# Optimization experiments

Hardware: AMD Instinct MI355X
Metric: run time of the kernel (lower is better)

## Reference

```python
import jax, jax.numpy as jnp
import numpy as np

N_NODES = 50000
N_EDGES = 800000
LATENT = 64
K_STEPS = 2
GAMMA = 0.9


def _xavier(key, fan_in, fan_out):
    lim = float(np.sqrt(6.0 / (fan_in + fan_out)))
    return jax.random.uniform(key, (fan_in, fan_out), minval=-lim, maxval=lim, dtype=jnp.float32)


def setup_inputs() -> dict:
    key = jax.random.key(0)
    ks = iter(jax.random.split(key, 48))
    L = LATENT
    inp = {}
    inp["x"] = jax.random.normal(next(ks), (N_NODES, 1), dtype=jnp.float32)
    inp["sol"] = jax.random.normal(next(ks), (N_NODES, 1), dtype=jnp.float32)
    inp["y"] = jax.random.normal(next(ks), (N_NODES, 1), dtype=jnp.float32)
    inp["tags"] = jax.random.randint(next(ks), (N_NODES,), 0, 2, dtype=jnp.int32)
    inp["edge_index"] = jax.random.randint(next(ks), (2, N_EDGES), 0, N_NODES, dtype=jnp.int32)
    inp["edge_attr"] = jax.random.normal(next(ks), (N_EDGES, 3), dtype=jnp.float32)
    inp["a_ij"] = jax.random.normal(next(ks), (N_EDGES,), dtype=jnp.float32)
    inp["prb_data"] = jax.random.normal(next(ks), (N_NODES, 2), dtype=jnp.float32)
    # phi_to / phi_from message MLPs: (2L+3) -> L -> L
    for name in ("pt", "pf"):
        inp[name + "_W1"] = _xavier(next(ks), 2 * L + 3, L)
        inp[name + "_b1"] = jnp.zeros((L,), jnp.float32)
        inp[name + "_W2"] = _xavier(next(ks), L, L)
        inp[name + "_b2"] = jnp.zeros((L,), jnp.float32)
    # gating MLPs: (3L+2) -> L, single linear + activation
    for name in ("zk", "rk", "corr"):
        inp[name + "_W"] = _xavier(next(ks), 3 * L + 2, L)
        inp[name + "_b"] = jnp.zeros((L,), jnp.float32)
    # encoder: 1 -> L -> L ; decoder: L -> L -> 1
    inp["e_W1"] = _xavier(next(ks), 1, L); inp["e_b1"] = jnp.zeros((L,), jnp.float32)
    inp["e_W2"] = _xavier(next(ks), L, L); inp["e_b2"] = jnp.zeros((L,), jnp.float32)
    inp["d_W1"] = _xavier(next(ks), L, L); inp["d_b1"] = jnp.zeros((L,), jnp.float32)
    inp["d_W2"] = _xavier(next(ks), L, 1); inp["d_b2"] = jnp.zeros((1,), jnp.float32)
    return inp


def reference(x, sol, y, tags, edge_index, edge_attr, a_ij, prb_data,
              pt_W1, pt_b1, pt_W2, pt_b2, pf_W1, pf_b1, pf_W2, pf_b2,
              zk_W, zk_b, rk_W, rk_b, corr_W, corr_b,
              e_W1, e_b1, e_W2, e_b2, d_W1, d_b1, d_W2, d_b2):
    n = x.shape[0]
    row, col = edge_index[0], edge_index[1]
    # remove_self_loops: mask out edges with row == col instead of slicing
    loop_mask = (row != col).astype(x.dtype)[:, None]

    def mlp2(t, W1, b1, W2, b2):  # Linear -> ReLU -> Linear
        return jnp.maximum(t @ W1 + b1, 0.0) @ W2 + b2

    def phi(h, i_idx, j_idx, W1, b1, W2, b2):
        # message = MLP([x_i, x_j, edge_attr]); aggr='add' at node i
        tmp = jnp.concatenate([h[i_idx], h[j_idx], edge_attr], axis=1)
        msg = mlp2(tmp, W1, b1, W2, b2) * loop_mask
        return jax.ops.segment_sum(msg, i_idx, num_segments=n)

    enc_p = (e_W1, e_b1, e_W2, e_b2)
    dec_p = (d_W1, d_b1, d_W2, d_b2)

    def apply(u, p):
        return mlp2(u, *p)

    def residual_loss(u):
        Au = jax.ops.segment_sum(a_ij[:, None] * u[col], row, num_segments=n)
        return jnp.mean((Au - y) ** 2)

    mse = lambda a, b: jnp.mean((a - b) ** 2)
    sg = lambda p: tuple(jax.lax.stop_gradient(t) for t in p)
    dir_mask = (tags == 1)[:, None]

    H0 = apply(x, enc_p)
    H = H0
    U = x
    total = jnp.float32(0.0)
    for step in range(K_STEPS):
        # phi_to: flow source->target => i = col (target); phi_from: i = row (source)
        mess_to = phi(H, col, row, pt_W1, pt_b1, pt_W2, pt_b2)
        mess_from = phi(H, row, col, pf_W1, pf_b1, pf_W2, pf_b2)
        cat = jnp.concatenate([H, mess_to, mess_from, prb_data], axis=1)
        alpha = jax.nn.sigmoid(cat @ zk_W + zk_b)
        reset = jax.nn.sigmoid(cat @ rk_W + rk_b)
        corr = jnp.tanh(
            jnp.concatenate([reset * H, mess_to, mess_from, prb_data], axis=1) @ corr_W + corr_b)
        Hn = H + alpha * corr
        Hn = jnp.where(dir_mask, H0, Hn)  # Dirichlet nodes reset to H['0']
        U = apply(Hn, dec_p)
        res = residual_loss(U)
        enc_loss = mse(apply(apply(Hn, sg(dec_p)), enc_p), Hn)        # 'latent'
        autoenc_loss = mse(apply(apply(U, sg(enc_p)), dec_p), U)      # 'physics'
        total = total + res * GAMMA ** (K_STEPS - step - 1) + enc_loss + autoenc_loss
        H = Hn
    return (U, total)
```

## Files before the change

### kernel.cpp

```cpp
#include <hip/hip_runtime.h>

#define DEV __device__ __forceinline__

constexpr int N = 50000;
constexpr int E = 800000;
constexpr int NBUK = 196;

constexpr int HF_OFF  = 0;
constexpr int H0F_OFF = 64*N;
constexpr int MTF_OFF = 128*N;
constexpr int MFF_OFF = 160*N;
constexpr int PBT_OFF = MTF_OFF;
constexpr int PBF_OFF = MFF_OFF;
constexpr int MP_OFF  = MTF_OFF;
constexpr int R1_OFF  = 192*N;
constexpr int PAT_OFF = R1_OFF;
constexpr int PAF_OFF = R1_OFF + 64*N;
constexpr int AL_OFF  = R1_OFF;
constexpr int RH_OFF  = R1_OFF + 64*N;
constexpr int T1_OFF  = R1_OFF;
constexpr int EV_OFF  = R1_OFF + 64*N;
constexpr int CSTG_OFF = R1_OFF;
constexpr int RSTG_OFF = R1_OFF + 4*E;
constexpr int HB_OFF   = 352*N;
constexpr int UV_OFF   = 384*N;
constexpr int LOSS_OFF = UV_OFF + N;
constexpr int FLAG_OFF = LOSS_OFF + 7;
constexpr int WZR_OFF = LOSS_OFF + 8;
constexpr int GB_OFF  = WZR_OFF + 24832;
constexpr int CW_OFF  = GB_OFF + 128;
constexpr int CB_OFF  = CW_OFF + 12416;
constexpr int PT1_OFF = CB_OFF + 64;
constexpr int AT_OFF  = PT1_OFF + 8192;
constexpr int BT1_OFF = AT_OFF + 192;
constexpr int WT2_OFF = BT1_OFF + 64;
constexpr int BT2_OFF = WT2_OFF + 4096;
constexpr int PF1_OFF = BT2_OFF + 64;
constexpr int AF_OFF  = PF1_OFF + 8192;
constexpr int BF1_OFF = AF_OFF + 192;
constexpr int WF2_OFF = BF1_OFF + 64;
constexpr int BF2_OFF = WF2_OFF + 4096;
constexpr int DW1_OFF = BF2_OFF + 64;
constexpr int DW2_OFF = DW1_OFF + 4096;
constexpr int DB1_OFF = DW2_OFF + 64;
constexpr int DB2_OFF = DB1_OFF + 64;
constexpr int EW1_OFF = DB2_OFF + 4;
constexpr int EB1_OFF = EW1_OFF + 64;
constexpr int EW2_OFF = EB1_OFF + 64;
constexpr int EB2_OFF = EW2_OFF + 4096;
constexpr int PRB0_OFF = EB2_OFF + 64;
constexpr int PRB1_OFF = PRB0_OFF + N;
constexpr int NWZR_OFF = PRB1_OFF + N;
constexpr int NCW_OFF  = NWZR_OFF + 25088;
constexpr int CNT_OFF  = NCW_OFF + 12544;
constexpr int FEND     = CNT_OFF + 2*N;
constexpr int CREC_OFF = FEND;
constexpr int RREC_OFF = CREC_OFF + 2*E;
constexpr int LCP_OFF  = RREC_OFF + 4*E;
constexpr int FRP_OFF  = LCP_OFF + N + 1;
constexpr int LE_OFF   = FRP_OFF + N + 1;
constexpr int LCF_OFF  = LE_OFF + N;
constexpr int LRF_OFF  = LCF_OFF + N;
constexpr int SFF_OFF  = LRF_OFF + N;
constexpr int CDEG_OFF = SFF_OFF + N;
constexpr int RDEG_OFF = CDEG_OFF + N;
constexpr int SDEG_OFF = RDEG_OFF + N;
constexpr int BS_OFF   = SDEG_OFF + N;
constexpr int BO_OFF   = BS_OFF + 512;
constexpr int GFC_OFF  = BO_OFF + 512;
constexpr int GFR_OFF  = GFC_OFF + 196;
constexpr int BKC_OFF  = GFR_OFF + 196;
constexpr int BKR_OFF  = BKC_OFF + 196;
constexpr int GBC_OFF  = BKR_OFF + 196;
constexpr int GBR_OFF  = GBC_OFF + 197;

constexpr int PREP_TOTAL = 24832+128+12416+64+8192+192+64+4096+64+8192+192+64+4096+64+4096+64+64+1+64+64+4096+64+6;
constexpr int PREP2_TOTAL = 25088 + 12544;

DEV float b2f(unsigned short u){ return __uint_as_float(((unsigned)u) << 16); }
DEV unsigned short f2b(float f){
    unsigned u = __float_as_uint(f);
    return (unsigned short)((u + 0x7fffu + ((u >> 16) & 1u)) >> 16);
}
DEV float blo(unsigned u){ return __uint_as_float(u << 16); }
DEV float bhi(unsigned u){ return __uint_as_float(u & 0xffff0000u); }
DEV int bcasti(int v, int k){ return __builtin_amdgcn_readlane(v, k); }
DEV float wave_sum(float v){
    #pragma unroll
    for (int off = 32; off > 0; off >>= 1) v += __shfl_xor(v, off, 64);
    return v;
}
DEV float ldv(const void* p, int i, bool isbf){
    return isbf ? b2f(((const unsigned short*)p)[i]) : ((const float*)p)[i];
}
DEV unsigned short ld16(const void* p, int i, bool isbf){
    return isbf ? ((const unsigned short*)p)[i] : f2b(((const float*)p)[i]);
}
DEV float sigm(float x){ return 1.f / (1.f + __expf(-x)); }

struct WPtrs {
    const void *ptW1, *ptb1, *ptW2, *ptb2;
    const void *pfW1, *pfb1, *pfW2, *pfb2;
    const void *zkW, *zkb, *rkW, *rkb, *cW, *cb;
    const void *eW1, *eb1, *eW2, *eb2;
    const void *dW1, *db1, *dW2, *db2;
};

__global__ __launch_bounds__(256) void detect_kernel(const void* y, float* __restrict__ ws){
    __shared__ int bad;
    if (threadIdx.x == 0) bad = 0;
    __syncthreads();
    const unsigned short* yy = (const unsigned short*)y;
    int mybad = 0;
    for (int i = threadIdx.x; i < 4096; i += 256){
        float v = b2f(yy[i]);
        if (!(v > -1.0e6f && v < 1.0e6f)) mybad = 1;
    }
    if (mybad) bad = 1;
    __syncthreads();
    if (threadIdx.x == 0) ws[FLAG_OFF] = bad ? 0.0f : 1.0f;
}

__global__ __launch_bounds__(256) void prep_kernel(WPtrs P, float* __restrict__ ws){
    int j = blockIdx.x * 256 + threadIdx.x;
    if (j >= PREP_TOTAL) return;
    bool isbf = ws[FLAG_OFF] > 0.5f;
    if (j < 24832){
        int k = j >> 7, c = j & 127;
        ws[WZR_OFF+j] = (c < 64) ? ldv(P.zkW, k*64+c, isbf) : ldv(P.rkW, k*64+(c-64), isbf);
        return;
    } j -= 24832;
    if (j < 128){ ws[GB_OFF+j] = (j < 64) ? ldv(P.zkb, j, isbf) : ldv(P.rkb, j-64, isbf); return; } j -= 128;
    if (j < 12416){ ws[CW_OFF+j] = ldv(P.cW, j, isbf); return; } j -= 12416;
    if (j < 64){ ws[CB_OFF+j] = ldv(P.cb, j, isbf); return; } j -= 64;
    if (j < 8192){ ws[PT1_OFF+j] = ldv(P.ptW1, j, isbf); return; } j -= 8192;
    if (j < 192){ ws[AT_OFF+j] = ldv(P.ptW1, 128*64+j, isbf); return; } j -= 192;
    if (j < 64){ ws[BT1_OFF+j] = ldv(P.ptb1, j, isbf); return; } j -= 64;
    if (j < 4096){ ws[WT2_OFF+j] = ldv(P.ptW2, j, isbf); return; } j -= 4096;
    if (j < 64){ ws[BT2_OFF+j] = ldv(P.ptb2, j, isbf); return; } j -= 64;
    if (j < 8192){ ws[PF1_OFF+j] = ldv(P.pfW1, j, isbf); return; } j -= 8192;
    if (j < 192){ ws[AF_OFF+j] = ldv(P.pfW1, 128*64+j, isbf); return; } j -= 192;
    if (j < 64){ ws[BF1_OFF+j] = ldv(P.pfb1, j, isbf); return; } j -= 64;
    if (j < 4096){ ws[WF2_OFF+j] = ldv(P.pfW2, j, isbf); return; } j -= 4096;
    if (j < 64){ ws[BF2_OFF+j] = ldv(P.pfb2, j, isbf); return; } j -= 64;
    if (j < 4096){ ws[DW1_OFF+j] = ldv(P.dW1, j, isbf); return; } j -= 4096;
    if (j < 64){ ws[DW2_OFF+j] = ldv(P.dW2, j, isbf); return; } j -= 64;
    if (j < 64){ ws[DB1_OFF+j] = ldv(P.db1, j, isbf); return; } j -= 64;
    if (j < 1){ ws[DB2_OFF] = ldv(P.db2, 0, isbf); return; } j -= 1;
    if (j < 64){ ws[EW1_OFF+j] = ldv(P.eW1, j, isbf); return; } j -= 64;
    if (j < 64){ ws[EB1_OFF+j] = ldv(P.eb1, j, isbf); return; } j -= 64;
    if (j < 4096){ ws[EW2_OFF+j] = ldv(P.eW2, j, isbf); return; } j -= 4096;
    if (j < 64){ ws[EB2_OFF+j] = ldv(P.eb2, j, isbf); return; } j -= 64;
    ws[LOSS_OFF+j] = 0.f;
}

__global__ __launch_bounds__(256) void prep2_kernel(float* __restrict__ ws){
    int j = blockIdx.x * 256 + threadIdx.x;
    if (j >= PREP2_TOTAL) return;
    if (j < 25088){
        int r = j >> 7, c = j & 127;
        float v;
        if (r < 64) v = ws[WZR_OFF + r*128 + c];
        else if (r < 128){
            int h = r - 64; float s = 0.f;
            for (int m = 0; m < 64; m++)
                s = fmaf(ws[WT2_OFF + h*64 + m], ws[WZR_OFF + (64+m)*128 + c], s);
            v = s;
        } else if (r < 192){
            int h = r - 128; float s = 0.f;
            for (int m = 0; m < 64; m++)
                s = fmaf(ws[WF2_OFF + h*64 + m], ws[WZR_OFF + (128+m)*128 + c], s);
            v = s;
        } else if (r < 194) v = ws[WZR_OFF + r*128 + c];
        else if (r == 194){
            float s = 0.f;
            for (int m = 0; m < 64; m++)
                s = fmaf(ws[BT2_OFF + m], ws[WZR_OFF + (64+m)*128 + c], s);
            v = s;
        } else {
            float s = 0.f;
            for (int m = 0; m < 64; m++)
                s = fmaf(ws[BF2_OFF + m], ws[WZR_OFF + (128+m)*128 + c], s);
            v = s;
        }
        ws[NWZR_OFF + j] = v;
        return;
    }
    j -= 25088;
    {
        int r = j >> 6, c = j & 63;
        float v;
        if (r < 64) v = ws[CW_OFF + r*64 + c];
        else if (r < 128){
            int h = r - 64; float s = 0.f;
            for (int m = 0; m < 64; m++)
                s = fmaf(ws[WT2_OFF + h*64 + m], ws[CW_OFF + (64+m)*64 + c], s);
            v = s;
        } else if (r < 192){
            int h = r - 128; float s = 0.f;
            for (int m = 0; m < 64; m++)
                s = fmaf(ws[WF2_OFF + h*64 + m], ws[CW_OFF + (128+m)*64 + c], s);
            v = s;
        } else if (r < 194) v = ws[CW_OFF + r*64 + c];
        else if (r == 194){
            float s = 0.f;
            for (int m = 0; m < 64; m++)
                s = fmaf(ws[BT2_OFF + m], ws[CW_OFF + (64+m)*64 + c], s);
            v = s;
        } else {
            float s = 0.f;
            for (int m = 0; m < 64; m++)
                s = fmaf(ws[BF2_OFF + m], ws[CW_OFF + (128+m)*64 + c], s);
            v = s;
        }
        ws[NCW_OFF + j] = v;
    }
}

__global__ __launch_bounds__(256) void setup_node(const void* __restrict__ prb, float* __restrict__ ws){
    int i = blockIdx.x * 256 + threadIdx.x;
    if (i >= N) return;
    bool isbf = ws[FLAG_OFF] > 0.5f;
    ws[PRB0_OFF+i] = ldv(prb, 2*i,   isbf);
    ws[PRB1_OFF+i] = ldv(prb, 2*i+1, isbf);
    if (i < NBUK){
        int* wsI = (int*)ws;
        wsI[BKC_OFF+i] = 0; wsI[BKR_OFF+i] = 0;
    }
}

__global__ __launch_bounds__(256) void bucket_hist(const int* __restrict__ ei, int* __restrict__ wsI){
    __shared__ int hc[NBUK], hr[NBUK];
    int t = threadIdx.x;
    for (int i = t; i < NBUK; i += 256){ hc[i] = 0; hr[i] = 0; }
    __syncthreads();
    int e0 = blockIdx.x * 4096;
    for (int i = 0; i < 16; i++){
        int e = e0 + i*256 + t;
        if (e < E){
            int r = ei[e], c = ei[E+e];
            if (r != c) atomicAdd(&hc[c >> 8], 1);
            atomicAdd(&hr[r >> 8], 1);
        }
    }
    __syncthreads();
    if (t < NBUK){
        if (hc[t]) atomicAdd(&wsI[BKC_OFF+t], hc[t]);
        if (hr[t]) atomicAdd(&wsI[BKR_OFF+t], hr[t]);
    }
}

__global__ __launch_bounds__(256) void bucket_scan(int* __restrict__ wsI){
    int y = blockIdx.y, t = threadIdx.x;
    const int* bk = wsI + (y ? BKR_OFF : BKC_OFF);
    int* gb = wsI + (y ? GBR_OFF : GBC_OFF);
    int* gf = wsI + (y ? GFR_OFF : GFC_OFF);
    __shared__ int sh[256];
    int v = (t < NBUK) ? bk[t] : 0;
    sh[t] = v;
    __syncthreads();
    #pragma unroll
    for (int off = 1; off < 256; off <<= 1){
        int u = (t >= (unsigned)off) ? sh[t - off] : 0;
        __syncthreads();
        sh[t] += u;
        __syncthreads();
    }
    int base = sh[t] - v;
    if (t < NBUK){ gb[t] = base; gf[t] = base; }
    if (t == NBUK - 1) gb[NBUK] = sh[t];
}

__global__ __launch_bounds__(256) void scatter_binA(const int* __restrict__ ei,
                                                    const void* __restrict__ attr,
                                                    const void* __restrict__ aij,
                                                    float* __restrict__ ws){
    __shared__ int hc[NBUK], hr[NBUK], bc[NBUK], br[NBUK];
    int t = threadIdx.x;
    for (int i = t; i < NBUK; i += 256){ hc[i] = 0; hr[i] = 0; }
    __syncthreads();
    int* wsI = (int*)ws;
    int e0 = blockIdx.x * 4096;
    for (int i = 0; i < 16; i++){
        int e = e0 + i*256 + t;
        if (e < E){
            int r = ei[e], c = ei[E+e];
            if (r != c) atomicAdd(&hc[c >> 8], 1);
            atomicAdd(&hr[r >> 8], 1);
        }
    }
    __syncthreads();
    if (t < NBUK){
        bc[t] = atomicAdd(&wsI[GFC_OFF+t], hc[t]);
        br[t] = atomicAdd(&wsI[GFR_OFF+t], hr[t]);
        hc[t] = 0; hr[t] = 0;
    }
    __syncthreads();
    bool isbf = ws[FLAG_OFF] > 0.5f;
    uint4* cstg = (uint4*)(ws + CSTG_OFF);
    uint4* rstg = (uint4*)(ws + RSTG_OFF);
    for (int i = 0; i < 16; i++){
        int e = e0 + i*256 + t;
        if (e < E){
            int r = ei[e], c = ei[E+e];
            unsigned a0 = ld16(attr, 3*e, isbf), a1 = ld16(attr, 3*e+1, isbf);
            unsigned a2 = ld16(attr, 3*e+2, isbf), av = ld16(aij, e, isbf);
            unsigned a01 = a0 | (a1 << 16);
            if (r != c){
                int off = atomicAdd(&hc[c >> 8], 1);
                cstg[bc[c >> 8] + off] = make_uint4((unsigned)r | (a2 << 16), a01, (unsigned)c, 0u);
            }
            int off2 = atomicAdd(&hr[r >> 8], 1);
            rstg[br[r >> 8] + off2] = make_uint4((unsigned)c | (a2 << 16), a01, av << 16, (unsigned)r);
        }
    }
}

__global__ __launch_bounds__(256) void deg_count(float* __restrict__ ws){
    __shared__ int cnt[256];
    __shared__ int scnt[256];
    int* wsI = (int*)ws;
    int b = blockIdx.x, t = threadIdx.x;
    cnt[t] = 0; scnt[t] = 0;
    __syncthreads();
    if (blockIdx.y == 0){
        int beg = wsI[GBC_OFF + b], end = wsI[GFC_OFF + b];
        const uint4* cstg = (const uint4*)(ws + CSTG_OFF);
        for (int p = beg + t; p < end; p += 256)
            atomicAdd(&cnt[(int)(cstg[p].z & 255u)], 1);
        __syncthreads();
        int node = b*256 + t;
        if (node < N) wsI[CDEG_OFF + node] = cnt[t];
    } else {
        int beg = wsI[GBR_OFF + b], end = wsI[GFR_OFF + b];
        const uint4* rstg = (const uint4*)(ws + RSTG_OFF);
        for (int p = beg + t; p < end; p += 256){
            uint4 q = rstg[p];
            int idx = (int)(q.w & 255u);
            atomicAdd(&cnt[idx], 1);
            if ((q.x & 0xffffu) == q.w) atomicAdd(&scnt[idx], 1);
        }
        __syncthreads();
        int node = b*256 + t;
        if (node < N){
            wsI[RDEG_OFF + node] = cnt[t];
            wsI[SDEG_OFF + node] = scnt[t];
        }
    }
}

DEV int deg_at(const int* wsI, int y, int i){
    if (y == 0) return wsI[CDEG_OFF+i];
    return wsI[RDEG_OFF+i];
}
__global__ __launch_bounds__(256) void scan1(int* __restrict__ wsI){
    int y = blockIdx.y;
    int* tmp = wsI + (y == 0 ? LCP_OFF : FRP_OFF);
    int i = blockIdx.x * 256 + threadIdx.x;
    __shared__ int sh[256];
    int v = (i < N) ? deg_at(wsI, y, i) : 0;
    sh[threadIdx.x] = v;
    __syncthreads();
    #pragma unroll
    for (int off = 1; off < 256; off <<= 1){
        int t = (threadIdx.x >= (unsigned)off) ? sh[threadIdx.x - off] : 0;
        __syncthreads();
        sh[threadIdx.x] += t;
        __syncthreads();
    }
    if (i < N) tmp[i] = sh[threadIdx.x] - v;
    if (threadIdx.x == 255) wsI[BS_OFF + y*256 + blockIdx.x] = sh[255];
}
__global__ __launch_bounds__(256) void scan2(int* __restrict__ wsI){
    int y = blockIdx.y, t = threadIdx.x;
    __shared__ int sh[256];
    int v = (t < 196) ? wsI[BS_OFF + y*256 + t] : 0;
    sh[t] = v;
    __syncthreads();
    #pragma unroll
    for (int off = 1; off < 256; off <<= 1){
        int u = (t >= (unsigned)off) ? sh[t - off] : 0;
        __syncthreads();
        sh[t] += u;
        __syncthreads();
    }
    wsI[BO_OFF + y*256 + t] = sh[t] - v;
}
__global__ __launch_bounds__(256) void scan3(int* __restrict__ wsI){
    int y = blockIdx.y;
    int* ptr = wsI + (y == 0 ? LCP_OFF : FRP_OFF);
    int i = blockIdx.x * 256 + threadIdx.x;
    if (i < N){
        int d = deg_at(wsI, y, i);
        int p = ptr[i] + wsI[BO_OFF + y*256 + blockIdx.x];
        ptr[i] = p;
        if (y == 0){
            wsI[LCF_OFF+i] = p;
            if (i == N-1) ptr[N] = p + d;
        } else {
            int live = wsI[RDEG_OFF+i] - wsI[SDEG_OFF+i];
            wsI[LRF_OFF+i] = p;
            wsI[LE_OFF+i]  = p + live;
            wsI[SFF_OFF+i] = p + live;
            if (i == N-1) ptr[N] = E;
        }
    }
}

__global__ __launch_bounds__(256) void scatter_binB(float* __restrict__ ws){
    int* wsI = (int*)ws;
    int b = blockIdx.x;
    if (blockIdx.y == 0){
        int beg = wsI[GBC_OFF + b];
        int end = wsI[GFC_OFF + b];
        const uint4* cstg = (const uint4*)(ws + CSTG_OFF);
        uint2* crec = (uint2*)(ws + CREC_OFF);
        for (int p = beg + threadIdx.x; p < end; p += 256){
            uint4 q = cstg[p];
            int d = atomicAdd(&wsI[LCF_OFF + (int)q.z], 1);
            crec[d] = make_uint2(q.x, q.y);
        }
    } else {
        int beg = wsI[GBR_OFF + b];
        int end = wsI[GFR_OFF + b];
        const uint4* rstg = (const uint4*)(ws + RSTG_OFF);
        uint4* rrec = (uint4*)(ws + RREC_OFF);
        for (int p = beg + threadIdx.x; p < end; p += 256){
            uint4 q = rstg[p];
            int r = (int)q.w;
            int c = (int)(q.x & 0xffffu);
            int d = (r != c) ? atomicAdd(&wsI[LRF_OFF + r], 1)
                             : atomicAdd(&wsI[SFF_OFF + r], 1);
            rrec[d] = make_uint4(q.x, q.y, q.z, 0u);
        }
    }
}

__global__ __launch_bounds__(256) void encode_init(const void* __restrict__ x,
                                                   float* __restrict__ ws){
    int node = blockIdx.x * 256 + threadIdx.x;
    if (node >= N) return;
    bool isbf = ws[FLAG_OFF] > 0.5f;
    int j0 = blockIdx.y * 32;
    float xv = ldv(x, node, isbf);
    float acc[32];
    #pragma unroll
    for (int j = 0; j < 32; j++) acc[j] = ws[EB2_OFF + j0 + j];
    for (int k = 0; k < 64; k++){
        float t = fmaxf(fmaf(xv, ws[EW1_OFF+k], ws[EB1_OFF+k]), 0.f);
        const float* wr = ws + EW2_OFF + (size_t)k*64 + j0;
        #pragma unroll
        for (int j = 0; j < 32; j++) acc[j] = fmaf(t, wr[j], acc[j]);
    }
    unsigned short* hb = (unsigned short*)(ws + HB_OFF);
    #pragma unroll
    for (int j = 0; j < 32; j++){
        ws[H0F_OFF + (size_t)(j0+j)*N + node] = acc[j];
        ws[HF_OFF  + (size_t)(j0+j)*N + node] = acc[j];
        hb[(size_t)(j0+j)*N + node] = f2b(acc[j]);
    }
}

__global__ __launch_bounds__(256) void node_pre(float* __restrict__ ws){
    int node = blockIdx.x * 256 + threadIdx.x;
    if (node >= N) return;
    int dir = blockIdx.y >> 2, tl = blockIdx.y & 3;
    int j0 = tl * 16;
    const float* W1 = ws + (dir ? PF1_OFF : PT1_OFF);
    float* paOut = ws + (dir ? PAF_OFF : PAT_OFF);
    unsigned short* pbOut = (unsigned short*)(ws + (dir ? PBF_OFF : PBT_OFF));
    const unsigned short* hb = (const unsigned short*)(ws + HB_OFF);
    float aA[16], aB[16];
    #pragma unroll
    for (int j = 0; j < 16; j++){ aA[j] = 0.f; aB[j] = 0.f; }
    #pragma unroll 4
    for (int k = 0; k < 64; k++){
        float hv = b2f(hb[(size_t)k*N + node]);
        const float* wA = W1 + (size_t)k*64 + j0;
        const float* wB = W1 + (size_t)(64+k)*64 + j0;
        #pragma unroll
        for (int j = 0; j < 16; j++){
            aA[j] = fmaf(hv, wA[j], aA[j]);
            aB[j] = fmaf(hv, wB[j], aB[j]);
        }
    }
    #pragma unroll
    for (int j = 0; j < 16; j++){
        paOut[(size_t)node*64 + j0 + j] = aA[j];
        pbOut[(size_t)node*64 + j0 + j] = f2b(aB[j]);
    }
}

template<int DIR>
__global__ __launch_bounds__(256) void gather_msgs(float* __restrict__ ws){
    const int* wsI = (const int*)ws;
    float* pa = ws + (DIR ? PAF_OFF : PAT_OFF);
    const unsigned short* pgb = (const unsigned short*)(ws + (DIR ? PBF_OFF : PBT_OFF));
    const float* A3 = ws + (DIR ? AF_OFF : AT_OFF);
    const float* b1 = ws + (DIR ? BF1_OFF : BT1_OFF);

    int lane = threadIdx.x & 63;
    int wv = threadIdx.x >> 6;
    float A0 = A3[lane], A1 = A3[64+lane], A2 = A3[128+lane];
    float B1 = b1[lane];
    int gw = blockIdx.x * 4 + wv;
    int nw = gridDim.x * 4;
    for (int node = gw; node < N; node += nw){
        float pav = pa[(size_t)node*64 + lane] + B1;
        float hs = 0.f;
        int beg, end;
        if (DIR == 0){ beg = wsI[LCP_OFF+node]; end = wsI[LCP_OFF+node+1]; }
        else         { beg = wsI[FRP_OFF+node]; end = wsI[LE_OFF+node]; }
        int cnt = end - beg;
        for (int base = beg; base < end; base += 64){
            int mcnt = end - base; if (mcnt > 64) mcnt = 64;
            unsigned rxL = 0, ryL = 0;
            if (lane < mcnt){
                if (DIR == 0){
                    uint2 q = ((const uint2*)(ws + CREC_OFF))[base + lane];
                    rxL = q.x; ryL = q.y;
                } else {
                    uint4 q = ((const uint4*)(ws + RREC_OFF))[base + lane];
                    rxL = q.x; ryL = q.y;
                }
            }
            for (int g = 0; g < mcnt; g += 8){
                unsigned rxa[8], rya[8];
                float pb[8];
                #pragma unroll
                for (int t = 0; t < 8; t++){
                    rxa[t] = (unsigned)bcasti((int)rxL, g+t);
                    rya[t] = (unsigned)bcasti((int)ryL, g+t);
                    int o = (int)(rxa[t] & 0xffffu);
                    float pv = b2f(pgb[(size_t)o*64 + lane]);
                    pb[t] = (g+t < mcnt) ? pv : -3.0e38f;
                }
                #pragma unroll
                for (int t = 0; t < 8; t++){
                    float hv = fmaf(blo(rya[t]), A0,
                               fmaf(bhi(rya[t]), A1,
                               fmaf(bhi(rxa[t]), A2, pav))) + pb[t];
                    hs += fmaxf(hv, 0.f);
                }
            }
        }
        pa[(size_t)node*64 + lane] = hs;
        if (lane == 0) ws[CNT_OFF + DIR*N + node] = (float)cnt;
    }
}

__global__ __launch_bounds__(256) void transpose_msg(float* __restrict__ ws){
    __shared__ float t[64][65];
    __shared__ float u[64][65];
    const float* srcT = ws + PAT_OFF;
    const float* srcF = ws + PAF_OFF;
    unsigned* mp = (unsigned*)(ws + MP_OFF);
    int n0 = blockIdx.x * 64;
    #pragma unroll
    for (int i = 0; i < 16; i++){
        int idx = i*256 + threadIdx.x;
        int nl = idx >> 6, f = idx & 63;
        int node = n0 + nl;
        t[nl][f] = (node < N) ? srcT[(size_t)node*64 + f] : 0.f;
        u[nl][f] = (node < N) ? srcF[(size_t)node*64 + f] : 0.f;
    }
    __syncthreads();
    #pragma unroll
    for (int i = 0; i < 16; i++){
        int idx = i*256 + threadIdx.x;
        int fw = idx >> 6, nl = idx & 63;
        int node = n0 + nl;
        if (node < N)
            mp[(size_t)fw*N + node] = (unsigned)f2b(t[nl][fw]) | ((unsigned)f2b(u[nl][fw]) << 16);
    }
}

__global__ __launch_bounds__(256) void gate_zr(float* __restrict__ ws){
    int node = blockIdx.x * 256 + threadIdx.x;
    if (node >= N) return;
    int tl = blockIdx.y, j0 = tl * 8;
    const float* W = ws + NWZR_OFF + j0;
    const unsigned short* hb = (const unsigned short*)(ws + HB_OFF);
    const unsigned* mp = (const unsigned*)(ws + MP_OFF);
    float p0 = ws[PRB0_OFF+node], p1 = ws[PRB1_OFF+node];
    float cT = ws[CNT_OFF+node], cF = ws[CNT_OFF+N+node];
    float az[8], ar[8];
    #pragma unroll
    for (int j = 0; j < 8; j++){
        az[j] = ws[GB_OFF + j0 + j]
              + p0*W[192*128+j] + p1*W[193*128+j] + cT*W[194*128+j] + cF*W[195*128+j];
        ar[j] = ws[GB_OFF + 64 + j0 + j]
              + p0*W[192*128+64+j] + p1*W[193*128+64+j] + cT*W[194*128+64+j] + cF*W[195*128+64+j];
    }
    #pragma unroll 4
    for (int k = 0; k < 64; k++){
        float aH = b2f(hb[(size_t)k*N + node]);
        unsigned m = mp[(size_t)k*N + node];
        float aT = blo(m), aF = bhi(m);
        const float* wH = W + (size_t)k*128;
        const float* wT = W + (size_t)(64+k)*128;
        const float* wF = W + (size_t)(128+k)*128;
        #pragma unroll
        for (int j = 0; j < 8; j++){
            az[j] = fmaf(aH, wH[j], fmaf(aT, wT[j], fmaf(aF, wF[j], az[j])));
            ar[j] = fmaf(aH, wH[64+j], fmaf(aT, wT[64+j], fmaf(aF, wF[64+j], ar[j])));
        }
    }
    unsigned short* RH = (unsigned short*)(ws + RH_OFF);
    #pragma unroll
    for (int j = 0; j < 8; j++){
        size_t off = (size_t)(j0+j)*N + node;
        ws[AL_OFF + off] = sigm(az[j]);
        RH[off] = f2b(sigm(ar[j]) * b2f(hb[off]));
    }
}

__global__ __launch_bounds__(256) void gate_corr(const int* __restrict__ tags,
                                                 float* __restrict__ ws){
    int node = blockIdx.x * 256 + threadIdx.x;
    if (node >= N) return;
    int tl = blockIdx.y, j0 = tl*8;
    const float* W = ws + NCW_OFF + j0;
    const unsigned short* RH = (const unsigned short*)(ws + RH_OFF);
    const unsigned* mp = (const unsigned*)(ws + MP_OFF);
    float p0 = ws[PRB0_OFF+node], p1 = ws[PRB1_OFF+node];
    float cT = ws[CNT_OFF+node], cF = ws[CNT_OFF+N+node];
    float acc[8];
    #pragma unroll
    for (int j = 0; j < 8; j++)
        acc[j] = ws[CB_OFF + j0 + j]
               + p0*W[192*64+j] + p1*W[193*64+j] + cT*W[194*64+j] + cF*W[195*64+j];
    #pragma unroll 4
    for (int k = 0; k < 64; k++){
        float aR = b2f(RH[(size_t)k*N + node]);
        unsigned m = mp[(size_t)k*N + node];
        float aT = blo(m), aF = bhi(m);
        const float* wR = W + (size_t)k*64;
        const float* wT = W + (size_t)(64+k)*64;
        const float* wF = W + (size_t)(128+k)*64;
        #pragma unroll
        for (int j = 0; j < 8; j++)
            acc[j] = fmaf(aR, wR[j], fmaf(aT, wT[j], fmaf(aF, wF[j], acc[j])));
    }
    int tg = tags[node];
    unsigned short* hb = (unsigned short*)(ws + HB_OFF);
    #pragma unroll
    for (int j = 0; j < 8; j++){
        size_t off = (size_t)(j0+j)*N + node;
        float hn = fmaf(ws[AL_OFF+off], tanhf(acc[j]), ws[HF_OFF+off]);
        if (tg == 1) hn = ws[H0F_OFF+off];
        ws[HF_OFF+off] = hn;
        hb[off] = f2b(hn);
    }
}

__global__ __launch_bounds__(256) void dec1hf(const unsigned short* __restrict__ src,
                                              float* __restrict__ dst,
                                              float* __restrict__ ws){
    int node = blockIdx.x * 256 + threadIdx.x;
    if (node >= N) return;
    int j0 = blockIdx.y * 16;
    float acc[16];
    #pragma unroll
    for (int j = 0; j < 16; j++) acc[j] = ws[DB1_OFF + j0 + j];
    #pragma unroll 4
    for (int k = 0; k < 64; k++){
        float a = b2f(src[(size_t)k*N + node]);
        const float* wr = ws + DW1_OFF + (size_t)k*64 + j0;
        #pragma unroll
        for (int j = 0; j < 16; j++) acc[j] = fmaf(a, wr[j], acc[j]);
    }
    #pragma unroll
    for (int j = 0; j < 16; j++)
        dst[(size_t)(j0+j)*N + node] = fmaxf(acc[j], 0.f);
}

__global__ __launch_bounds__(256) void dec1hb(const unsigned short* __restrict__ src,
                                              unsigned short* __restrict__ dst,
                                              float* __restrict__ ws){
    int node = blockIdx.x * 256 + threadIdx.x;
    if (node >= N) return;
    int j0 = blockIdx.y * 16;
    float acc[16];
    #pragma unroll
    for (int j = 0; j < 16; j++) acc[j] = ws[DB1_OFF + j0 + j];
    #pragma unroll 4
    for (int k = 0; k < 64; k++){
        float a = b2f(src[(size_t)k*N + node]);
        const float* wr = ws + DW1_OFF + (size_t)k*64 + j0;
        #pragma unroll
        for (int j = 0; j < 16; j++) acc[j] = fmaf(a, wr[j], acc[j]);
    }
    #pragma unroll
    for (int j = 0; j < 16; j++)
        dst[(size_t)(j0+j)*N + node] = f2b(fmaxf(acc[j], 0.f));
}

__global__ __launch_bounds__(256) void calc_u(float* __restrict__ ws){
    int node = blockIdx.x * 256 + threadIdx.x;
    if (node >= N) return;
    const float* T1 = ws + T1_OFF;
    float u0 = 0.f, u1 = 0.f, u2 = 0.f, u3 = 0.f;
    #pragma unroll 4
    for (int j = 0; j < 16; j++){
        u0 = fmaf(T1[(size_t)(4*j  )*N + node], ws[DW2_OFF + 4*j  ], u0);
        u1 = fmaf(T1[(size_t)(4*j+1)*N + node], ws[DW2_OFF + 4*j+1], u1);
        u2 = fmaf(T1[(size_t)(4*j+2)*N + node], ws[DW2_OFF + 4*j+2], u2);
        u3 = fmaf(T1[(size_t)(4*j+3)*N + node], ws[DW2_OFF + 4*j+3], u3);
    }
    ws[UV_OFF+node] = (u0 + u1) + (u2 + u3) + ws[DB2_OFF];
}

__global__ __launch_bounds__(256) void enc_u(int step, float* __restrict__ ws){
    int node = blockIdx.x * 256 + threadIdx.x;
    float encA = 0.f;
    if (node < N){
        int j0 = blockIdx.y * 16;
        float u = ws[UV_OFF+node];
        float acc[16];
        #pragma unroll
        for (int j = 0; j < 16; j++) acc[j] = ws[EB2_OFF + j0 + j];
        for (int k = 0; k < 64; k++){
            float t = fmaxf(fmaf(u, ws[EW1_OFF+k], ws[EB1_OFF+k]), 0.f);
            const float* wr = ws + EW2_OFF + (size_t)k*64 + j0;
            #pragma unroll
            for (int j = 0; j < 16; j++) acc[j] = fmaf(t, wr[j], acc[j]);
        }
        unsigned short* ev = (unsigned short*)(ws + EV_OFF);
        #pragma unroll
        for (int j = 0; j < 16; j++){
            size_t off = (size_t)(j0+j)*N + node;
            ev[off] = f2b(acc[j]);
            float d = acc[j] - ws[HF_OFF+off];
            encA += d*d;
        }
    }
    encA = wave_sum(encA);
    if ((threadIdx.x & 63) == 0) atomicAdd(&ws[LOSS_OFF + step*3 + 1], encA);
}

__global__ __launch_bounds__(256) void aux_res(int step, const void* __restrict__ y,
                                               float* __restrict__ ws){
    const int* wsI = (const int*)ws;
    int node = blockIdx.x * 256 + threadIdx.x;
    bool isbf = ws[FLAG_OFF] > 0.5f;
    float autoA = 0.f, resA = 0.f;
    if (node < N){
        const unsigned short* T1u = (const unsigned short*)(ws + T1_OFF);
        float u0 = 0.f, u1 = 0.f, u2s = 0.f, u3 = 0.f;
        #pragma unroll 4
        for (int j = 0; j < 16; j++){
            u0  = fmaf(b2f(T1u[(size_t)(4*j  )*N + node]), ws[DW2_OFF + 4*j  ], u0);
            u1  = fmaf(b2f(T1u[(size_t)(4*j+1)*N + node]), ws[DW2_OFF + 4*j+1], u1);
            u2s = fmaf(b2f(T1u[(size_t)(4*j+2)*N + node]), ws[DW2_OFF + 4*j+2], u2s);
            u3  = fmaf(b2f(T1u[(size_t)(4*j+3)*N + node]), ws[DW2_OFF + 4*j+3], u3);
        }
        float u2 = (u0 + u1) + (u2s + u3) + ws[DB2_OFF];
        float u = ws[UV_OFF+node];
        float ad = u2 - u;
        autoA = ad*ad;
        float acc = 0.f;
        int beg = wsI[FRP_OFF+node], end = wsI[FRP_OFF+node+1];
        const uint4* rrec = (const uint4*)(ws + RREC_OFF);
        for (int p = beg; p < end; p++){
            uint4 q = rrec[p];
            acc = fmaf(bhi(q.z), ws[UV_OFF + (int)(q.x & 0xffffu)], acc);
        }
        float d = acc - ldv(y, node, isbf);
        resA = d*d;
    }
    autoA = wave_sum(autoA);
    resA = wave_sum(resA);
    if ((threadIdx.x & 63) == 0){
        atomicAdd(&ws[LOSS_OFF + step*3 + 2], autoA);
        atomicAdd(&ws[LOSS_OFF + step*3], resA);
    }
}

__global__ __launch_bounds__(256) void write_out(void* __restrict__ outp,
                                                 const float* __restrict__ ws){
    int i = blockIdx.x * 256 + threadIdx.x;
    if (i > N) return;
    bool isbf = ws[FLAG_OFF] > 0.5f;
    float v;
    if (i < N){
        v = ws[UV_OFF+i];
    } else {
        const float* L = ws + LOSS_OFF;
        float inv = 1.f / (float)N, invl = 1.f / ((float)N * 64.f);
        v = 0.9f*L[0]*inv + L[1]*invl + L[2]*inv
          +      L[3]*inv + L[4]*invl + L[5]*inv;
    }
    if (isbf) ((unsigned short*)outp)[i] = f2b(v);
    else      ((float*)outp)[i] = v;
}

extern "C" void kernel_launch(void* const* d_in, const int* in_sizes, int n_in,
                              void* d_out, int out_size, void* d_ws, size_t ws_size,
                              hipStream_t stream){
    const void* x    = d_in[0];
    const void* y    = d_in[2];
    const int* tags  = (const int*)d_in[3];
    const int* ei    = (const int*)d_in[4];
    const void* attr = d_in[5];
    const void* aij  = d_in[6];
    const void* prb  = d_in[7];
    WPtrs P;
    P.ptW1 = d_in[8];  P.ptb1 = d_in[9];  P.ptW2 = d_in[10]; P.ptb2 = d_in[11];
    P.pfW1 = d_in[12]; P.pfb1 = d_in[13]; P.pfW2 = d_in[14]; P.pfb2 = d_in[15];
    P.zkW  = d_in[16]; P.zkb  = d_in[17]; P.rkW  = d_in[18]; P.rkb  = d_in[19];
    P.cW   = d_in[20]; P.cb   = d_in[21];
    P.eW1  = d_in[22]; P.eb1  = d_in[23]; P.eW2  = d_in[24]; P.eb2  = d_in[25];
    P.dW1  = d_in[26]; P.db1  = d_in[27]; P.dW2  = d_in[28]; P.db2  = d_in[29];
    float* ws = (float*)d_ws;
    int* wsI = (int*)d_ws;

    detect_kernel<<<1, 256, 0, stream>>>(y, ws);
    prep_kernel<<<(PREP_TOTAL + 255)/256, 256, 0, stream>>>(P, ws);
    prep2_kernel<<<(PREP2_TOTAL + 255)/256, 256, 0, stream>>>(ws);
    setup_node<<<196, 256, 0, stream>>>(prb, ws);
    bucket_hist<<<196, 256, 0, stream>>>(ei, wsI);
    bucket_scan<<<dim3(1, 2), 256, 0, stream>>>(wsI);
    scatter_binA<<<196, 256, 0, stream>>>(ei, attr, aij, ws);
    deg_count<<<dim3(196, 2), 256, 0, stream>>>(ws);
    scan1<<<dim3(196, 2), 256, 0, stream>>>(wsI);
    scan2<<<dim3(1, 2), 256, 0, stream>>>(wsI);
    scan3<<<dim3(196, 2), 256, 0, stream>>>(wsI);
    scatter_binB<<<dim3(196, 2), 256, 0, stream>>>(ws);
    encode_init<<<dim3(196, 2), 256, 0, stream>>>(x, ws);
    unsigned short* hb = (unsigned short*)(ws + HB_OFF);
    unsigned short* ev = (unsigned short*)(ws + EV_OFF);
    for (int step = 0; step < 2; step++){
        node_pre<<<dim3(196, 8), 256, 0, stream>>>(ws);
        gather_msgs<0><<<2048, 256, 0, stream>>>(ws);
        gather_msgs<1><<<2048, 256, 0, stream>>>(ws);
        transpose_msg<<<782, 256, 0, stream>>>(ws);
        gate_zr<<<dim3(196, 8), 256, 0, stream>>>(ws);
        gate_corr<<<dim3(196, 8), 256, 0, stream>>>(tags, ws);
        dec1hf<<<dim3(196, 4), 256, 0, stream>>>(hb, ws + T1_OFF, ws);
        calc_u<<<196, 256, 0, stream>>>(ws);
        enc_u<<<dim3(196, 4), 256, 0, stream>>>(step, ws);
        dec1hb<<<dim3(196, 4), 256, 0, stream>>>(ev, (unsigned short*)(ws + T1_OFF), ws);
        aux_res<<<196, 256, 0, stream>>>(step, y, ws);
    }
    write_out<<<197, 256, 0, stream>>>(d_out, ws);
}
```

Baseline: 831.6 us.

## Replace scalar-input encoder MLP with piecewise-linear lookup tables

The encoder takes a scalar input, so its 1->64 ReLU -> 64 layer is piecewise linear in that input, with breakpoints at -b1/w1. A new one-block prep kernel sorts those breakpoints and precomputes slope and intercept vectors for each of the 65 segments. encode_init and enc_u then count how many breakpoints lie below the input and do one fma per output instead of a 64x64 loop. This removes most of the encoder arithmetic, but adds a small serial prep kernel and can round slightly differently from the original.

```diff
diff --git a/kernel.cpp b/kernel.cpp
--- a/kernel.cpp
+++ b/kernel.cpp
@@ -73,6 +73,9 @@
 constexpr int BKR_OFF  = BKC_OFF + 196;
 constexpr int GBC_OFF  = BKR_OFF + 196;
 constexpr int GBR_OFF  = GBC_OFF + 197;
+constexpr int ENCT_OFF = GBR_OFF + 197;
+constexpr int ENCA_OFF = ENCT_OFF + 64;
+constexpr int ENCB_OFF = ENCA_OFF + 4160;
 
 constexpr int PREP_TOTAL = 24832+128+12416+64+8192+192+64+4096+64+8192+192+64+4096+64+4096+64+64+1+64+64+4096+64+6;
 constexpr int PREP2_TOTAL = 25088 + 12544;
@@ -217,6 +220,45 @@
     }
 }
 
+__global__ void prep3_kernel(float* __restrict__ ws){
+    __shared__ float tb[64];
+    __shared__ int srt[64];
+    int t = threadIdx.x;
+    float w1 = ws[EW1_OFF + t], b1 = ws[EB1_OFF + t];
+    float tk = (w1 != 0.f) ? (-b1 / w1) : 3.0e38f;
+    tb[t] = tk;
+    __syncthreads();
+    int rank = 0;
+    for (int j = 0; j < 64; j++){
+        float tj = tb[j];
+        if (tj < tk || (tj == tk && j < t)) rank++;
+    }
+    srt[rank] = t;
+    __syncthreads();
+    ws[ENCT_OFF + t] = tb[srt[t]];
+    int j = t;
+    float A = 0.f, B = ws[EB2_OFF + j];
+    for (int k = 0; k < 64; k++){
+        float w = ws[EW1_OFF+k], b = ws[EB1_OFF+k];
+        if (w < 0.f || (w == 0.f && b > 0.f)){
+            float e2 = ws[EW2_OFF + k*64 + j];
+            A += w * e2;
+            B += b * e2;
+        }
+    }
+    for (int m = 0; m <= 64; m++){
+        ws[ENCA_OFF + m*64 + j] = A;
+        ws[ENCB_OFF + m*64 + j] = B;
+        if (m < 64){
+            int k = srt[m];
+            float w = ws[EW1_OFF+k], b = ws[EB1_OFF+k];
+            float e2 = ws[EW2_OFF + k*64 + j];
+            if (w > 0.f){ A += w*e2; B += b*e2; }
+            else if (w < 0.f){ A -= w*e2; B -= b*e2; }
+        }
+    }
+}
+
 __global__ __launch_bounds__(256) void setup_node(const void* __restrict__ prb, float* __restrict__ ws){
     int i = blockIdx.x * 256 + threadIdx.x;
     if (i >= N) return;
@@ -443,21 +485,18 @@
     bool isbf = ws[FLAG_OFF] > 0.5f;
     int j0 = blockIdx.y * 32;
     float xv = ldv(x, node, isbf);
-    float acc[32];
-    #pragma unroll
-    for (int j = 0; j < 32; j++) acc[j] = ws[EB2_OFF + j0 + j];
-    for (int k = 0; k < 64; k++){
-        float t = fmaxf(fmaf(xv, ws[EW1_OFF+k], ws[EB1_OFF+k]), 0.f);
-        const float* wr = ws + EW2_OFF + (size_t)k*64 + j0;
-        #pragma unroll
-        for (int j = 0; j < 32; j++) acc[j] = fmaf(t, wr[j], acc[j]);
-    }
+    int m = 0;
+    #pragma unroll 8
+    for (int i = 0; i < 64; i++) m += (ws[ENCT_OFF+i] < xv) ? 1 : 0;
+    const float* Av = ws + ENCA_OFF + m*64 + j0;
+    const float* Bv = ws + ENCB_OFF + m*64 + j0;
     unsigned short* hb = (unsigned short*)(ws + HB_OFF);
     #pragma unroll
     for (int j = 0; j < 32; j++){
-        ws[H0F_OFF + (size_t)(j0+j)*N + node] = acc[j];
-        ws[HF_OFF  + (size_t)(j0+j)*N + node] = acc[j];
-        hb[(size_t)(j0+j)*N + node] = f2b(acc[j]);
+        float a = fmaf(xv, Av[j], Bv[j]);
+        ws[H0F_OFF + (size_t)(j0+j)*N + node] = a;
+        ws[HF_OFF  + (size_t)(j0+j)*N + node] = a;
+        hb[(size_t)(j0+j)*N + node] = f2b(a);
     }
 }
 
@@ -717,21 +756,18 @@
     if (node < N){
         int j0 = blockIdx.y * 16;
         float u = ws[UV_OFF+node];
-        float acc[16];
-        #pragma unroll
-        for (int j = 0; j < 16; j++) acc[j] = ws[EB2_OFF + j0 + j];
-        for (int k = 0; k < 64; k++){
-            float t = fmaxf(fmaf(u, ws[EW1_OFF+k], ws[EB1_OFF+k]), 0.f);
-            const float* wr = ws + EW2_OFF + (size_t)k*64 + j0;
-            #pragma unroll
-            for (int j = 0; j < 16; j++) acc[j] = fmaf(t, wr[j], acc[j]);
-        }
+        int m = 0;
+        #pragma unroll 8
+        for (int i = 0; i < 64; i++) m += (ws[ENCT_OFF+i] < u) ? 1 : 0;
+        const float* Av = ws + ENCA_OFF + m*64 + j0;
+        const float* Bv = ws + ENCB_OFF + m*64 + j0;
         unsigned short* ev = (unsigned short*)(ws + EV_OFF);
         #pragma unroll
         for (int j = 0; j < 16; j++){
+            float e = fmaf(u, Av[j], Bv[j]);
             size_t off = (size_t)(j0+j)*N + node;
-            ev[off] = f2b(acc[j]);
-            float d = acc[j] - ws[HF_OFF+off];
+            ev[off] = f2b(e);
+            float d = e - ws[HF_OFF+off];
             encA += d*d;
         }
     }
@@ -818,6 +854,7 @@
     detect_kernel<<<1, 256, 0, stream>>>(y, ws);
     prep_kernel<<<(PREP_TOTAL + 255)/256, 256, 0, stream>>>(P, ws);
     prep2_kernel<<<(PREP2_TOTAL + 255)/256, 256, 0, stream>>>(ws);
+    prep3_kernel<<<1, 64, 0, stream>>>(ws);
     setup_node<<<196, 256, 0, stream>>>(prb, ws);
     bucket_hist<<<196, 256, 0, stream>>>(ei, wsI);
     bucket_scan<<<dim3(1, 2), 256, 0, stream>>>(wsI);
```

Measured after the change: 862.0 us. +3.7%, slower.
